# Optimization experiments

Measured on AMD Instinct MI355X. Metric: run time of the kernel, lower is better.

The kernel has to match this reference:

```python
import jax, jax.numpy as jnp
import numpy as np

DT = 0.02          # full control timestep (cfg dt)
N_SUBSTEPS = 8     # RK4 substeps per forward call
LMBDA = 0.5        # first-order actuator lag gain
G_VEC = jnp.array([0.0, 0.0, -9.81], dtype=jnp.float32)
N_ENVS = 2097152


def setup_inputs() -> dict:
    key = jax.random.key(0)
    k1, k2 = jax.random.split(key)
    X0 = jax.random.normal(k1, (N_ENVS, 9), dtype=jnp.float32)
    U = jax.random.normal(k2, (N_ENVS, 3), dtype=jnp.float32)
    return {"X0": X0, "U": U}


def reference(X0, U):
    h = DT / N_SUBSTEPS  # substep size

    def dynamics(X):
        v = X[:, 3:6]
        a = X[:, 6:9]
        a_dot = LMBDA * (U - a) / DT   # actuator lag uses full dt, as in torch code
        # X_dot = [p_dot, v_dot, a_dot] = [v, a - g_vec, a_dot]
        return jnp.concatenate([v, a - G_VEC, a_dot], axis=-1)

    def rk4_step(X, _):
        k1 = dynamics(X)
        k2 = dynamics(X + 0.5 * h * k1)
        k3 = dynamics(X + 0.5 * h * k2)
        k4 = dynamics(X + h * k3)
        X_next = X + (h / 6.0) * (k1 + 2.0 * k2 + 2.0 * k3 + k4)
        return X_next, None

    X_final, _ = jax.lax.scan(rk4_step, X0, None, length=N_SUBSTEPS)
    return X_final
```

## Files before the change

### kernel.cpp

```cpp
#include <hip/hip_runtime.h>


#define ENVS_PER_BLOCK 256
#define THREADS 256

struct Coeffs {
    float P00, P01, P02;
    float P10, P11, P12;
    float P20, P21, P22;
    float Ku0, Ku1, Ku2;
    float Kg0, Kg1, Kg2;
};

__global__ __launch_bounds__(THREADS)
void pointmass_kernel(const float* __restrict__ X0,
                      const float* __restrict__ U,
                      float* __restrict__ Out,
                      int envTotal, Coeffs cf) {
    __shared__ float s_x[ENVS_PER_BLOCK * 9];
    __shared__ float s_u[ENVS_PER_BLOCK * 3];

    const int t = threadIdx.x;
    const int blockBase = blockIdx.x * ENVS_PER_BLOCK;
    const int envsHere = min(ENVS_PER_BLOCK, envTotal - blockBase);

    if (envsHere == ENVS_PER_BLOCK) {
        const float4* x4 = (const float4*)(X0 + (size_t)blockBase * 9);
        const float4* u4 = (const float4*)(U  + (size_t)blockBase * 3);
        float4* o4 = (float4*)(Out + (size_t)blockBase * 9);

        #pragma unroll
        for (int j = t; j < ENVS_PER_BLOCK * 9 / 4; j += THREADS)
            ((float4*)s_x)[j] = x4[j];
        if (t < ENVS_PER_BLOCK * 3 / 4)
            ((float4*)s_u)[t] = u4[t];
        __syncthreads();

        float r[9];
        #pragma unroll
        for (int k = 0; k < 3; ++k) {
            const float p = s_x[t * 9 + k];
            const float v = s_x[t * 9 + 3 + k];
            const float a = s_x[t * 9 + 6 + k];
            const float u = s_u[t * 3 + k];
            const float g = (k == 2) ? -9.81f : 0.0f;
            r[k]     = cf.P00 * p + cf.P01 * v + cf.P02 * a + cf.Ku0 * u + cf.Kg0 * g;
            r[3 + k] = cf.P10 * p + cf.P11 * v + cf.P12 * a + cf.Ku1 * u + cf.Kg1 * g;
            r[6 + k] = cf.P20 * p + cf.P21 * v + cf.P22 * a + cf.Ku2 * u + cf.Kg2 * g;
        }
        #pragma unroll
        for (int i = 0; i < 9; ++i) s_x[t * 9 + i] = r[i];
        __syncthreads();

        #pragma unroll
        for (int j = t; j < ENVS_PER_BLOCK * 9 / 4; j += THREADS)
            o4[j] = ((const float4*)s_x)[j];
    } else {
        for (int j = t; j < envsHere * 9; j += THREADS)
            s_x[j] = X0[(size_t)blockBase * 9 + j];
        for (int j = t; j < envsHere * 3; j += THREADS)
            s_u[j] = U[(size_t)blockBase * 3 + j];
        __syncthreads();
        if (t < envsHere) {
            float r[9];
            #pragma unroll
            for (int k = 0; k < 3; ++k) {
                const float p = s_x[t * 9 + k];
                const float v = s_x[t * 9 + 3 + k];
                const float a = s_x[t * 9 + 6 + k];
                const float u = s_u[t * 3 + k];
                const float g = (k == 2) ? -9.81f : 0.0f;
                r[k]     = cf.P00 * p + cf.P01 * v + cf.P02 * a + cf.Ku0 * u + cf.Kg0 * g;
                r[3 + k] = cf.P10 * p + cf.P11 * v + cf.P12 * a + cf.Ku1 * u + cf.Kg1 * g;
                r[6 + k] = cf.P20 * p + cf.P21 * v + cf.P22 * a + cf.Ku2 * u + cf.Kg2 * g;
            }
            #pragma unroll
            for (int i = 0; i < 9; ++i)
                Out[((size_t)blockBase + t) * 9 + i] = r[i];
        }
    }
}

static void mat3_mul(const double A[3][3], const double B[3][3], double C[3][3]) {
    for (int i = 0; i < 3; ++i)
        for (int j = 0; j < 3; ++j) {
            double s = 0.0;
            for (int k = 0; k < 3; ++k) s += A[i][k] * B[k][j];
            C[i][j] = s;
        }
}
static void mat3_copy(const double A[3][3], double B[3][3]) {
    for (int i = 0; i < 3; ++i) for (int j = 0; j < 3; ++j) B[i][j] = A[i][j];
}

extern "C" void kernel_launch(void* const* d_in, const int* in_sizes, int n_in,
                              void* d_out, int out_size, void* d_ws, size_t ws_size,
                              hipStream_t stream) {
    const float* X0 = (const float*)d_in[0];
    const float* U  = (const float*)d_in[1];
    float* Out = (float*)d_out;
    const int envTotal = in_sizes[0] / 9;

    const double DT = 0.02;
    const double h = DT / 8.0;
    const double c = 0.5 / DT;
    double hA[3][3] = {{0, h, 0}, {0, 0, h}, {0, 0, -c * h}};

    double hA2[3][3], hA3[3][3], hA4[3][3];
    mat3_mul(hA, hA, hA2);
    mat3_mul(hA2, hA, hA3);
    mat3_mul(hA3, hA, hA4);

    double P[3][3], Q[3][3];
    for (int i = 0; i < 3; ++i)
        for (int j = 0; j < 3; ++j) {
            const double I = (i == j) ? 1.0 : 0.0;
            P[i][j] = I + hA[i][j] + hA2[i][j] / 2.0 + hA3[i][j] / 6.0 + hA4[i][j] / 24.0;
            Q[i][j] = h * (I + hA[i][j] / 2.0 + hA2[i][j] / 6.0 + hA3[i][j] / 24.0);
        }

    double P2[3][3], P4[3][3], P8[3][3];
    mat3_mul(P, P, P2);
    mat3_mul(P2, P2, P4);
    mat3_mul(P4, P4, P8);

    double IP[3][3], IP2[3][3], IP4[3][3], T[3][3], S[3][3], R[3][3];
    mat3_copy(P, IP);  mat3_copy(P2, IP2);  mat3_copy(P4, IP4);
    for (int i = 0; i < 3; ++i) { IP[i][i] += 1.0; IP2[i][i] += 1.0; IP4[i][i] += 1.0; }
    mat3_mul(IP, IP2, T);
    mat3_mul(T, IP4, S);
    mat3_mul(S, Q, R);

    Coeffs cf;
    cf.P00 = (float)P8[0][0]; cf.P01 = (float)P8[0][1]; cf.P02 = (float)P8[0][2];
    cf.P10 = (float)P8[1][0]; cf.P11 = (float)P8[1][1]; cf.P12 = (float)P8[1][2];
    cf.P20 = (float)P8[2][0]; cf.P21 = (float)P8[2][1]; cf.P22 = (float)P8[2][2];
    cf.Ku0 = (float)(R[0][2] * c); cf.Ku1 = (float)(R[1][2] * c); cf.Ku2 = (float)(R[2][2] * c);
    cf.Kg0 = (float)(-R[0][1]);    cf.Kg1 = (float)(-R[1][1]);    cf.Kg2 = (float)(-R[2][1]);

    const int blocks = (envTotal + ENVS_PER_BLOCK - 1) / ENVS_PER_BLOCK;
    pointmass_kernel<<<blocks, THREADS, 0, stream>>>(X0, U, Out, envTotal, cf);
}
```

Baseline: 154.2 us.

## Process four tiles per block with double-buffered LDS prefetch of next tile

Each block now handles a chunk of four 256-env tiles rather than one. While the current tile is computed and stored, the loads for the next tile are issued into registers and then written into the second LDS buffer. A custom barrier waits only on LDS counters. The aim is to overlap global-memory latency with compute and store and to cut block launch overhead, at the cost of a quarter as many blocks and extra synchronization per tile.

```diff
diff --git a/kernel.cpp b/kernel.cpp
--- a/kernel.cpp
+++ b/kernel.cpp
@@ -1,8 +1,9 @@
 #include <hip/hip_runtime.h>
 
 
-#define ENVS_PER_BLOCK 256
 #define THREADS 256
+#define TILE 256
+#define CHUNK 4
 
 struct Coeffs {
     float P00, P01, P02;
@@ -12,71 +13,124 @@
     float Kg0, Kg1, Kg2;
 };
 
+__device__ __forceinline__ void barrier_lgkm() {
+    asm volatile("s_waitcnt lgkmcnt(0)" ::: "memory");
+    __builtin_amdgcn_s_barrier();
+    asm volatile("" ::: "memory");
+}
+
+__device__ __forceinline__ void compute_env(const float* __restrict__ sx,
+                                            const float* __restrict__ su,
+                                            const Coeffs& cf, float r[9]) {
+    #pragma unroll
+    for (int k = 0; k < 3; ++k) {
+        const float p = sx[k];
+        const float v = sx[3 + k];
+        const float a = sx[6 + k];
+        const float u = su[k];
+        const float g = (k == 2) ? -9.81f : 0.0f;
+        r[k]     = cf.P00 * p + cf.P01 * v + cf.P02 * a + cf.Ku0 * u + cf.Kg0 * g;
+        r[3 + k] = cf.P10 * p + cf.P11 * v + cf.P12 * a + cf.Ku1 * u + cf.Kg1 * g;
+        r[6 + k] = cf.P20 * p + cf.P21 * v + cf.P22 * a + cf.Ku2 * u + cf.Kg2 * g;
+    }
+}
+
 __global__ __launch_bounds__(THREADS)
 void pointmass_kernel(const float* __restrict__ X0,
                       const float* __restrict__ U,
                       float* __restrict__ Out,
                       int envTotal, Coeffs cf) {
-    __shared__ float s_x[ENVS_PER_BLOCK * 9];
-    __shared__ float s_u[ENVS_PER_BLOCK * 3];
+    __shared__ float s_x[2][TILE * 9];
+    __shared__ float s_u[2][TILE * 3];
 
     const int t = threadIdx.x;
-    const int blockBase = blockIdx.x * ENVS_PER_BLOCK;
-    const int envsHere = min(ENVS_PER_BLOCK, envTotal - blockBase);
+    const int tileTotal = (envTotal + TILE - 1) / TILE;
+    const int tb = blockIdx.x * CHUNK;
+    if (tb >= tileTotal) return;
+    const int te = min(tb + CHUNK, tileTotal);
 
-    if (envsHere == ENVS_PER_BLOCK) {
-        const float4* x4 = (const float4*)(X0 + (size_t)blockBase * 9);
-        const float4* u4 = (const float4*)(U  + (size_t)blockBase * 3);
-        float4* o4 = (float4*)(Out + (size_t)blockBase * 9);
+    const bool allFull = (te * TILE <= envTotal);
 
-        #pragma unroll
-        for (int j = t; j < ENVS_PER_BLOCK * 9 / 4; j += THREADS)
-            ((float4*)s_x)[j] = x4[j];
-        if (t < ENVS_PER_BLOCK * 3 / 4)
-            ((float4*)s_u)[t] = u4[t];
-        __syncthreads();
+    if (allFull) {
+        const float4* X4 = (const float4*)X0;
+        const float4* U4 = (const float4*)U;
+        float4* O4 = (float4*)Out;
 
-        float r[9];
-        #pragma unroll
-        for (int k = 0; k < 3; ++k) {
-            const float p = s_x[t * 9 + k];
-            const float v = s_x[t * 9 + 3 + k];
-            const float a = s_x[t * 9 + 6 + k];
-            const float u = s_u[t * 3 + k];
-            const float g = (k == 2) ? -9.81f : 0.0f;
-            r[k]     = cf.P00 * p + cf.P01 * v + cf.P02 * a + cf.Ku0 * u + cf.Kg0 * g;
-            r[3 + k] = cf.P10 * p + cf.P11 * v + cf.P12 * a + cf.Ku1 * u + cf.Kg1 * g;
-            r[6 + k] = cf.P20 * p + cf.P21 * v + cf.P22 * a + cf.Ku2 * u + cf.Kg2 * g;
+        {
+            const size_t xb = (size_t)tb * 576;
+            const size_t ub = (size_t)tb * 192;
+            float4 a0 = X4[xb + t];
+            float4 a1 = X4[xb + t + 256];
+            float4 a2 = make_float4(0.f, 0.f, 0.f, 0.f);
+            float4 b0 = make_float4(0.f, 0.f, 0.f, 0.f);
+            if (t < 64)  a2 = X4[xb + t + 512];
+            if (t < 192) b0 = U4[ub + t];
+            ((float4*)s_x[0])[t]       = a0;
+            ((float4*)s_x[0])[t + 256] = a1;
+            if (t < 64)  ((float4*)s_x[0])[t + 512] = a2;
+            if (t < 192) ((float4*)s_u[0])[t]       = b0;
         }
-        #pragma unroll
-        for (int i = 0; i < 9; ++i) s_x[t * 9 + i] = r[i];
-        __syncthreads();
+        barrier_lgkm();
 
-        #pragma unroll
-        for (int j = t; j < ENVS_PER_BLOCK * 9 / 4; j += THREADS)
-            o4[j] = ((const float4*)s_x)[j];
+        int cur = 0;
+        for (int i = tb; i < te; ++i) {
+            const bool haveNext = (i + 1 < te);
+
+            float4 a0, a1;
+            float4 a2 = make_float4(0.f, 0.f, 0.f, 0.f);
+            float4 b0 = make_float4(0.f, 0.f, 0.f, 0.f);
+            if (haveNext) {
+                const size_t xb = (size_t)(i + 1) * 576;
+                const size_t ub = (size_t)(i + 1) * 192;
+                a0 = X4[xb + t];
+                a1 = X4[xb + t + 256];
+                if (t < 64)  a2 = X4[xb + t + 512];
+                if (t < 192) b0 = U4[ub + t];
+            }
+
+            {
+                float r[9];
+                compute_env(s_x[cur] + t * 9, s_u[cur] + t * 3, cf, r);
+                float* sxw = s_x[cur] + t * 9;
+                #pragma unroll
+                for (int q = 0; q < 9; ++q) sxw[q] = r[q];
+            }
+            barrier_lgkm();
+
+            {
+                const size_t ob = (size_t)i * 576;
+                O4[ob + t]       = ((const float4*)s_x[cur])[t];
+                O4[ob + t + 256] = ((const float4*)s_x[cur])[t + 256];
+                if (t < 64) O4[ob + t + 512] = ((const float4*)s_x[cur])[t + 512];
+            }
+
+            if (haveNext) {
+                const int nxt = cur ^ 1;
+                ((float4*)s_x[nxt])[t]       = a0;
+                ((float4*)s_x[nxt])[t + 256] = a1;
+                if (t < 64)  ((float4*)s_x[nxt])[t + 512] = a2;
+                if (t < 192) ((float4*)s_u[nxt])[t]       = b0;
+                barrier_lgkm();
+                cur = nxt;
+            }
+        }
     } else {
-        for (int j = t; j < envsHere * 9; j += THREADS)
-            s_x[j] = X0[(size_t)blockBase * 9 + j];
-        for (int j = t; j < envsHere * 3; j += THREADS)
-            s_u[j] = U[(size_t)blockBase * 3 + j];
-        __syncthreads();
-        if (t < envsHere) {
-            float r[9];
-            #pragma unroll
-            for (int k = 0; k < 3; ++k) {
-                const float p = s_x[t * 9 + k];
-                const float v = s_x[t * 9 + 3 + k];
-                const float a = s_x[t * 9 + 6 + k];
-                const float u = s_u[t * 3 + k];
-                const float g = (k == 2) ? -9.81f : 0.0f;
-                r[k]     = cf.P00 * p + cf.P01 * v + cf.P02 * a + cf.Ku0 * u + cf.Kg0 * g;
-                r[3 + k] = cf.P10 * p + cf.P11 * v + cf.P12 * a + cf.Ku1 * u + cf.Kg1 * g;
-                r[6 + k] = cf.P20 * p + cf.P21 * v + cf.P22 * a + cf.Ku2 * u + cf.Kg2 * g;
+        for (int i = tb; i < te; ++i) {
+            const int base = i * TILE;
+            const int n = min(TILE, envTotal - base);
+            __syncthreads();
+            for (int j = t; j < n * 9; j += THREADS)
+                s_x[0][j] = X0[(size_t)base * 9 + j];
+            for (int j = t; j < n * 3; j += THREADS)
+                s_u[0][j] = U[(size_t)base * 3 + j];
+            __syncthreads();
+            if (t < n) {
+                float r[9];
+                compute_env(s_x[0] + t * 9, s_u[0] + t * 3, cf, r);
+                #pragma unroll
+                for (int q = 0; q < 9; ++q)
+                    Out[((size_t)base + t) * 9 + q] = r[q];
             }
-            #pragma unroll
-            for (int i = 0; i < 9; ++i)
-                Out[((size_t)blockBase + t) * 9 + i] = r[i];
         }
     }
 }
@@ -138,6 +192,7 @@
     cf.Ku0 = (float)(R[0][2] * c); cf.Ku1 = (float)(R[1][2] * c); cf.Ku2 = (float)(R[2][2] * c);
     cf.Kg0 = (float)(-R[0][1]);    cf.Kg1 = (float)(-R[1][1]);    cf.Kg2 = (float)(-R[2][1]);
 
-    const int blocks = (envTotal + ENVS_PER_BLOCK - 1) / ENVS_PER_BLOCK;
+    const int tileTotal = (envTotal + TILE - 1) / TILE;
+    const int blocks = (tileTotal + CHUNK - 1) / CHUNK;
     pointmass_kernel<<<blocks, THREADS, 0, stream>>>(X0, U, Out, envTotal, cf);
 }
```

After: 157.0 us. Within noise of the previous version (+1.8%).
